# Kernel tuning notes

Hardware: AMD Instinct MI355X
Metric: run time of the kernel (lower is better)

The kernel has to match this reference:

```python
import jax, jax.numpy as jnp
import numpy as np

N, L, HID = 8192, 256, 128   # rows, input_len, hidden_size
H, NLIN = 2, 2               # n_heads, n_linear
EPS = 1e-5


def setup_inputs() -> dict:
    key = jax.random.key(0)
    ks = jax.random.split(key, 8)
    # attention params (torch.randn in source; scaled 0.02 for numerical sanity of softmax logits)
    Q = jax.random.normal(ks[0], (H, L, HID), jnp.float32) * 0.02
    K = jax.random.normal(ks[1], (H, L, HID), jnp.float32) * 0.02
    V_down = jax.random.normal(ks[2], (H, L, HID), jnp.float32) * 0.02
    V_up = jax.random.normal(ks[3], (H, HID, L), jnp.float32) * 0.02
    # nn.Linear(input_len, input_len): uniform(-1/sqrt(L), 1/sqrt(L))
    bnd = 1.0 / np.sqrt(L)
    W = jax.random.uniform(ks[4], (NLIN, L, L), jnp.float32, -bnd, bnd)
    b = jax.random.uniform(ks[5], (NLIN, L), jnp.float32, -bnd, bnd)
    x = jax.random.normal(ks[6], (N, L), jnp.float32)
    return {"x": x, "Q": Q, "K": K, "V_down": V_down, "V_up": V_up, "W": W, "b": b}


def _batch_norm(z):
    # custom BatchNorm1d: per-feature normalization over the batch (row) dim, no affine
    m = jnp.mean(z, axis=0, keepdims=True)
    v = jnp.var(z, axis=0, keepdims=True)
    return (z - m) * jax.lax.rsqrt(v + EPS)


def reference(x, Q, K, V_down, V_up, W, b):
    h = _batch_norm(x)                              # [N, L]
    dE = jnp.zeros_like(h)
    for i in range(Q.shape[0]):                     # small fixed head count
        q = h @ Q[i]                                # [N, HID]
        k = h @ K[i]                                # [N, HID]
        A = jax.nn.softmax(q @ k.T, axis=1)         # [N, N]
        dE = dE + A @ (h @ V_down[i]) @ V_up[i]     # low-rank value path
    h = _batch_norm(h + dE)
    for j in range(W.shape[0]):                     # per-row Linear+ReLU loop == batched matmul
        h = jax.nn.relu(h @ W[j].T + b[j])
    return h
```

## Files before the change

### kernel.cpp

```cpp
#include <hip/hip_runtime.h>
#include <hip/hip_bf16.h>

constexpr int Nrows = 8192;
constexpr int L     = 256;
constexpr int D     = 128;
constexpr float EPS = 1e-5f;

typedef __bf16 bf16x8 __attribute__((ext_vector_type(8)));
typedef __bf16 bf16x4 __attribute__((ext_vector_type(4)));
typedef float  f32x4  __attribute__((ext_vector_type(4)));

#define MFMA16(a, b, c) __builtin_amdgcn_mfma_f32_16x16x32_bf16((a), (b), (c), 0, 0, 0)

__global__ void k_cvt_params(const float* __restrict__ Q, const float* __restrict__ K,
                             const float* __restrict__ Vd, const float* __restrict__ Vup,
                             const float* __restrict__ W,
                             __bf16* __restrict__ Bt, __bf16* __restrict__ VupT,
                             __bf16* __restrict__ Wb) {
    int i = blockIdx.x * 256 + threadIdx.x;
    if (i < 6 * 128 * 256) {
        int g = i >> 15; int r = i & 32767; int d = r >> 8; int l = r & 255;
        const float* src = (g % 3 == 0 ? Q : (g % 3 == 1 ? K : Vd)) + (g / 3) * (L * D);
        Bt[i] = (__bf16)src[l * D + d];
    } else if (i < 8 * 128 * 256) {
        int j = i - 6 * 128 * 256;
        int h = j >> 15; int r = j & 32767; int l = r >> 7; int d = r & 127;
        VupT[j] = (__bf16)Vup[h * (D * L) + d * L + l];
    } else {
        int j = i - 8 * 128 * 256;
        Wb[j] = (__bf16)W[j];
    }
}

__global__ void k_bn_stats(const float* __restrict__ x, float* __restrict__ sum,
                           float* __restrict__ sq) {
    int col = threadIdx.x;
    int r0 = blockIdx.x * 64;
    float s = 0.f, s2 = 0.f;
    for (int i = 0; i < 64; i++) {
        float v = x[(r0 + i) * L + col];
        s += v; s2 += v * v;
    }
    atomicAdd(&sum[col], s);
    atomicAdd(&sq[col], s2);
}

__global__ void k_bn_norm1(const float* __restrict__ x, const float* __restrict__ sum,
                           const float* __restrict__ sq, __bf16* __restrict__ hb,
                           float* __restrict__ hf) {
    int i = (blockIdx.x * 256 + threadIdx.x) * 4;
    int col = i & (L - 1);
    f32x4 v = *(const f32x4*)(x + i);
    bf16x4 o; f32x4 of;
#pragma unroll
    for (int j = 0; j < 4; j++) {
        float m   = sum[col + j] * (1.0f / Nrows);
        float var = sq[col + j] * (1.0f / Nrows) - m * m;
        float rs  = rsqrtf(var + EPS);
        float t = (v[j] - m) * rs;
        of[j] = t; o[j] = (__bf16)t;
    }
    *(bf16x4*)(hb + i) = o;
    *(f32x4*)(hf + i) = of;
}

__global__ void k_bn_norm2(const float* __restrict__ z, const float* __restrict__ sum,
                           const float* __restrict__ sq, __bf16* __restrict__ h) {
    int i = (blockIdx.x * 256 + threadIdx.x) * 4;
    int col = i & (L - 1);
    f32x4 v = *(const f32x4*)(z + i);
    bf16x4 o;
#pragma unroll
    for (int j = 0; j < 4; j++) {
        float m   = sum[col + j] * (1.0f / Nrows);
        float var = sq[col + j] * (1.0f / Nrows) - m * m;
        float rs  = rsqrtf(var + EPS);
        o[j] = (__bf16)((v[j] - m) * rs);
    }
    *(bf16x4*)(h + i) = o;
}

__launch_bounds__(256)
__global__ void k_gemm_qkv(const __bf16* __restrict__ h, const __bf16* __restrict__ Bt,
                           __bf16* __restrict__ q0, __bf16* __restrict__ k0,
                           __bf16* __restrict__ q1, __bf16* __restrict__ k1,
                           __bf16* __restrict__ Vt) {
    int g = blockIdx.y;
    int m0 = blockIdx.x * 128;
    int w = threadIdx.x >> 6, lane = threadIdx.x & 63;
    int c = lane & 15, qd = lane >> 4;
    int mw = m0 + w * 32;
    const __bf16* B = Bt + g * (128 * 256);

    f32x4 acc[2][8] = {};
#pragma unroll
    for (int kc = 0; kc < 8; kc++) {
        bf16x8 a0 = *(const bf16x8*)(h + (mw + c) * L + kc * 32 + qd * 8);
        bf16x8 a1 = *(const bf16x8*)(h + (mw + 16 + c) * L + kc * 32 + qd * 8);
#pragma unroll
        for (int nt = 0; nt < 8; nt++) {
            bf16x8 b = *(const bf16x8*)(B + (nt * 16 + c) * L + kc * 32 + qd * 8);
            acc[0][nt] = MFMA16(a0, b, acc[0][nt]);
            acc[1][nt] = MFMA16(a1, b, acc[1][nt]);
        }
    }
    if (g == 2 || g == 5) {
        __bf16* vt = Vt + (g / 3) * (128 * Nrows);
#pragma unroll
        for (int mt = 0; mt < 2; mt++)
#pragma unroll
            for (int nt = 0; nt < 8; nt++)
#pragma unroll
                for (int r = 0; r < 4; r++) {
                    int row = mw + mt * 16 + 4 * qd + r;
                    int colv = nt * 16 + c;
                    vt[colv * Nrows + row] = (__bf16)acc[mt][nt][r];
                }
    } else {
        __bf16* dst = (g == 0) ? q0 : (g == 1) ? k0 : (g == 3) ? q1 : k1;
#pragma unroll
        for (int mt = 0; mt < 2; mt++)
#pragma unroll
            for (int nt = 0; nt < 8; nt++)
#pragma unroll
                for (int r = 0; r < 4; r++) {
                    int row = mw + mt * 16 + 4 * qd + r;
                    int colv = nt * 16 + c;
                    dst[row * D + colv] = (__bf16)acc[mt][nt][r];
                }
    }
}

__launch_bounds__(256, 1)
__global__ void k_flash(const __bf16* __restrict__ q0, const __bf16* __restrict__ k0,
                        const __bf16* __restrict__ q1, const __bf16* __restrict__ k1,
                        const __bf16* __restrict__ Vt, __bf16* __restrict__ O) {
    int head = blockIdx.x & 1;
    int qtile = blockIdx.x >> 1;
    int m0 = qtile * 64;
    const __bf16* qm = head ? q1 : q0;
    const __bf16* km = head ? k1 : k0;
    const __bf16* vt = Vt + head * (128 * Nrows);
    __bf16* Og = O + head * (Nrows * D);

    int w = threadIdx.x >> 6, lane = threadIdx.x & 63;
    int c = lane & 15, qd = lane >> 4;

    __shared__ __bf16 Pb[4][64 * 56];
    __shared__ float l_red[4][64];
    __shared__ float l_inv[64];
    __shared__ float obuf[4][64][16];

    bf16x8 aq[4][4];
#pragma unroll
    for (int mt = 0; mt < 4; mt++)
#pragma unroll
        for (int kc = 0; kc < 4; kc++)
            aq[mt][kc] = *(const bf16x8*)(qm + (m0 + mt * 16 + c) * D + kc * 32 + qd * 8);

    f32x4 oacc[4][8] = {};
    float lp[4][4] = {};
    __bf16* Pw = &Pb[w][0];

    auto loadkv = [&](bf16x8 (&kb)[2][4], bf16x8 (&vb)[8], int n0) {
        int nb = n0 + w * 32;
#pragma unroll
        for (int nt = 0; nt < 2; nt++)
#pragma unroll
            for (int kc = 0; kc < 4; kc++)
                kb[nt][kc] = *(const bf16x8*)(km + (nb + nt * 16 + c) * D + kc * 32 + qd * 8);
#pragma unroll
        for (int dvt = 0; dvt < 8; dvt++)
            vb[dvt] = *(const bf16x8*)(vt + (dvt * 16 + c) * Nrows + nb + qd * 8);
    };

    auto compute = [&](const bf16x8 (&kb)[2][4], const bf16x8 (&vb)[8]) {
#pragma unroll
        for (int nt = 0; nt < 2; nt++) {
            f32x4 s[4] = {};
            __builtin_amdgcn_s_setprio(1);
#pragma unroll
            for (int kc = 0; kc < 4; kc++) {
#pragma unroll
                for (int mt = 0; mt < 4; mt++) s[mt] = MFMA16(aq[mt][kc], kb[nt][kc], s[mt]);
            }
            __builtin_amdgcn_s_setprio(0);
#pragma unroll
            for (int mt = 0; mt < 4; mt++)
#pragma unroll
                for (int r = 0; r < 4; r++) {
                    float e = __expf(s[mt][r]);
                    lp[mt][r] += e;
                    Pw[(mt * 16 + 4 * qd + r) * 56 + nt * 16 + c] = (__bf16)e;
                }
        }
        bf16x8 ap[4];
#pragma unroll
        for (int mt = 0; mt < 4; mt++)
            ap[mt] = *(const bf16x8*)(Pw + (mt * 16 + c) * 56 + qd * 8);
        __builtin_amdgcn_s_setprio(1);
#pragma unroll
        for (int dvt = 0; dvt < 8; dvt++) {
#pragma unroll
            for (int mt = 0; mt < 4; mt++) oacc[mt][dvt] = MFMA16(ap[mt], vb[dvt], oacc[mt][dvt]);
        }
        __builtin_amdgcn_s_setprio(0);
    };

    bf16x8 kbA[2][4], vbA[8], kbB[2][4], vbB[8];
    loadkv(kbA, vbA, 0);
    for (int n0 = 0; n0 < Nrows; n0 += 256) {
        loadkv(kbB, vbB, n0 + 128);
        compute(kbA, vbA);
        if (n0 + 256 < Nrows)
            loadkv(kbA, vbA, n0 + 256);
        compute(kbB, vbB);
    }

#pragma unroll
    for (int mt = 0; mt < 4; mt++)
#pragma unroll
        for (int r = 0; r < 4; r++) {
            float v = lp[mt][r];
            v += __shfl_xor(v, 1, 16);
            v += __shfl_xor(v, 2, 16);
            v += __shfl_xor(v, 4, 16);
            v += __shfl_xor(v, 8, 16);
            lp[mt][r] = v;
        }
    if (c == 0) {
#pragma unroll
        for (int mt = 0; mt < 4; mt++)
#pragma unroll
            for (int r = 0; r < 4; r++)
                l_red[w][mt * 16 + 4 * qd + r] = lp[mt][r];
    }
    __syncthreads();
    if (threadIdx.x < 64)
        l_inv[threadIdx.x] = 1.0f / (l_red[0][threadIdx.x] + l_red[1][threadIdx.x] +
                                     l_red[2][threadIdx.x] + l_red[3][threadIdx.x]);

    for (int dvt = 0; dvt < 8; dvt++) {
        __syncthreads();
#pragma unroll
        for (int mt = 0; mt < 4; mt++)
#pragma unroll
            for (int r = 0; r < 4; r++)
                obuf[w][mt * 16 + 4 * qd + r][c] = oacc[mt][dvt][r];
        __syncthreads();
        int t = threadIdx.x;
        int row = (t * 4) >> 4, col = (t * 4) & 15;
        f32x4 v = *(const f32x4*)&obuf[0][row][col];
        f32x4 v1 = *(const f32x4*)&obuf[1][row][col];
        f32x4 v2 = *(const f32x4*)&obuf[2][row][col];
        f32x4 v3 = *(const f32x4*)&obuf[3][row][col];
        float il = l_inv[row];
        bf16x4 o;
#pragma unroll
        for (int e = 0; e < 4; e++) o[e] = (__bf16)((v[e] + v1[e] + v2[e] + v3[e]) * il);
        *(bf16x4*)(Og + (m0 + row) * D + dvt * 16 + col) = o;
    }
}

__launch_bounds__(256)
__global__ void k_gemm_vup(const __bf16* __restrict__ O, const __bf16* __restrict__ VupT,
                           const float* __restrict__ hf, float* __restrict__ z) {
    int n0 = blockIdx.y * 128;
    int m0 = blockIdx.x * 128;
    int w = threadIdx.x >> 6, lane = threadIdx.x & 63;
    int c = lane & 15, qd = lane >> 4;
    int mw = m0 + w * 32;

    f32x4 acc[2][8] = {};
#pragma unroll
    for (int kc = 0; kc < 8; kc++) {
        const __bf16* Oh = O + (kc >> 2) * (Nrows * D);
        const __bf16* Vh = VupT + (kc >> 2) * (L * D);
        int ko = (kc & 3) * 32 + qd * 8;
        bf16x8 a0 = *(const bf16x8*)(Oh + (mw + c) * D + ko);
        bf16x8 a1 = *(const bf16x8*)(Oh + (mw + 16 + c) * D + ko);
#pragma unroll
        for (int nt = 0; nt < 8; nt++) {
            bf16x8 b = *(const bf16x8*)(Vh + (n0 + nt * 16 + c) * D + ko);
            acc[0][nt] = MFMA16(a0, b, acc[0][nt]);
            acc[1][nt] = MFMA16(a1, b, acc[1][nt]);
        }
    }
#pragma unroll
    for (int mt = 0; mt < 2; mt++)
#pragma unroll
        for (int nt = 0; nt < 8; nt++)
#pragma unroll
            for (int r = 0; r < 4; r++) {
                int row = mw + mt * 16 + 4 * qd + r;
                int col = n0 + nt * 16 + c;
                z[row * L + col] = acc[mt][nt][r] + hf[row * L + col];
            }
}

template <typename OutT>
__launch_bounds__(256)
__global__ void k_gemm_w(const __bf16* __restrict__ hin, const __bf16* __restrict__ W,
                         const float* __restrict__ bias, OutT* __restrict__ out) {
    int n0 = blockIdx.y * 128;
    int m0 = blockIdx.x * 128;
    int w = threadIdx.x >> 6, lane = threadIdx.x & 63;
    int c = lane & 15, qd = lane >> 4;
    int mw = m0 + w * 32;

    f32x4 acc[2][8] = {};
#pragma unroll
    for (int kc = 0; kc < 8; kc++) {
        bf16x8 a0 = *(const bf16x8*)(hin + (mw + c) * L + kc * 32 + qd * 8);
        bf16x8 a1 = *(const bf16x8*)(hin + (mw + 16 + c) * L + kc * 32 + qd * 8);
#pragma unroll
        for (int nt = 0; nt < 8; nt++) {
            bf16x8 b = *(const bf16x8*)(W + (n0 + nt * 16 + c) * L + kc * 32 + qd * 8);
            acc[0][nt] = MFMA16(a0, b, acc[0][nt]);
            acc[1][nt] = MFMA16(a1, b, acc[1][nt]);
        }
    }
#pragma unroll
    for (int mt = 0; mt < 2; mt++)
#pragma unroll
        for (int nt = 0; nt < 8; nt++) {
            int col = n0 + nt * 16 + c;
            float bv = bias[col];
#pragma unroll
            for (int r = 0; r < 4; r++) {
                int row = mw + mt * 16 + 4 * qd + r;
                float v = fmaxf(acc[mt][nt][r] + bv, 0.0f);
                out[row * L + col] = (OutT)v;
            }
        }
}

extern "C" void kernel_launch(void* const* d_in, const int* in_sizes, int n_in,
                              void* d_out, int out_size, void* d_ws, size_t ws_size,
                              hipStream_t stream) {
    (void)in_sizes; (void)n_in; (void)out_size; (void)ws_size;
    const float* x   = (const float*)d_in[0];
    const float* Q   = (const float*)d_in[1];
    const float* K   = (const float*)d_in[2];
    const float* Vd  = (const float*)d_in[3];
    const float* Vup = (const float*)d_in[4];
    const float* W   = (const float*)d_in[5];
    const float* b   = (const float*)d_in[6];
    float* out = (float*)d_out;

    char* ws = (char*)d_ws;
    size_t off = 0;
    auto alloc = [&](size_t bytes) -> void* {
        void* p = ws + off;
        off += (bytes + 255) & ~(size_t)255;
        return p;
    };
    float*  stats = (float*)alloc(4 * 256 * sizeof(float));
    __bf16* Bt    = (__bf16*)alloc(6 * 128 * 256 * 2);
    __bf16* VupT  = (__bf16*)alloc(2 * 256 * 128 * 2);
    __bf16* Wb    = (__bf16*)alloc(2 * 256 * 256 * 2);
    __bf16* hb    = (__bf16*)alloc((size_t)Nrows * L * 2);
    float*  hf    = (float*)alloc((size_t)Nrows * L * 4);
    __bf16* q0    = (__bf16*)alloc((size_t)Nrows * D * 2);
    __bf16* k0    = (__bf16*)alloc((size_t)Nrows * D * 2);
    __bf16* q1    = (__bf16*)alloc((size_t)Nrows * D * 2);
    __bf16* k1    = (__bf16*)alloc((size_t)Nrows * D * 2);
    __bf16* Vt    = (__bf16*)alloc((size_t)2 * 128 * Nrows * 2);
    __bf16* O     = (__bf16*)alloc((size_t)2 * Nrows * D * 2);
    float*  z     = (float*)alloc((size_t)Nrows * L * 4);
    __bf16* h2    = (__bf16*)alloc((size_t)Nrows * L * 2);
    __bf16* h3    = (__bf16*)alloc((size_t)Nrows * L * 2);

    float* sum1 = stats, *sq1 = stats + 256, *sum2 = stats + 512, *sq2 = stats + 768;

    hipMemsetAsync(stats, 0, 4 * 256 * sizeof(float), stream);
    k_cvt_params<<<1536, 256, 0, stream>>>(Q, K, Vd, Vup, W, Bt, VupT, Wb);
    k_bn_stats<<<128, 256, 0, stream>>>(x, sum1, sq1);
    k_bn_norm1<<<2048, 256, 0, stream>>>(x, sum1, sq1, hb, hf);
    k_gemm_qkv<<<dim3(64, 6), 256, 0, stream>>>(hb, Bt, q0, k0, q1, k1, Vt);
    k_flash<<<256, 256, 0, stream>>>(q0, k0, q1, k1, Vt, O);
    k_gemm_vup<<<dim3(64, 2), 256, 0, stream>>>(O, VupT, hf, z);
    k_bn_stats<<<128, 256, 0, stream>>>(z, sum2, sq2);
    k_bn_norm2<<<2048, 256, 0, stream>>>(z, sum2, sq2, h2);
    k_gemm_w<__bf16><<<dim3(64, 2), 256, 0, stream>>>(h2, Wb, b, h3);
    k_gemm_w<float><<<dim3(64, 2), 256, 0, stream>>>(h3, Wb + 256 * 256, b + 256, out);
}
```

Baseline: 306.0 us.

## Keep softmax probabilities in registers via transposed QK^T and K16 MFMA for PV

Restructures the attention kernel so S^T is computed as K·Q^T, whose accumulator layout matches the B operand of a 16x16x16 bf16 MFMA. The exponentiated probabilities then feed the PV product straight from registers instead of making a round trip through shared memory. Work is split across 8 waves, each owning 16 query rows and half of every 64-key chunk, and the two halves are reduced in shared memory at the end. This removes the LDS write/read of P, but each wave reloads K/V for fewer query rows (less reuse per load) and uses a smaller-K MFMA.

```diff
diff --git a/kernel.cpp b/kernel.cpp
--- a/kernel.cpp
+++ b/kernel.cpp
@@ -9,8 +9,15 @@
 typedef __bf16 bf16x8 __attribute__((ext_vector_type(8)));
 typedef __bf16 bf16x4 __attribute__((ext_vector_type(4)));
 typedef float  f32x4  __attribute__((ext_vector_type(4)));
+typedef short  s16x4  __attribute__((ext_vector_type(4)));
 
 #define MFMA16(a, b, c) __builtin_amdgcn_mfma_f32_16x16x32_bf16((a), (b), (c), 0, 0, 0)
+
+#if __has_builtin(__builtin_amdgcn_mfma_f32_16x16x16bf16_1k)
+#define MFMA_K16(A_, B_, C_) (C_) = __builtin_amdgcn_mfma_f32_16x16x16bf16_1k((A_), (B_), (C_), 0, 0, 0)
+#else
+#define MFMA_K16(A_, B_, C_) asm volatile("s_nop 1\n\tv_mfma_f32_16x16x16_bf16 %0, %1, %2, %0" : "+v"(C_) : "v"(A_), "v"(B_))
+#endif
 
 __global__ void k_cvt_params(const float* __restrict__ Q, const float* __restrict__ K,
                              const float* __restrict__ Vd, const float* __restrict__ Vup,
@@ -131,7 +138,7 @@
     }
 }
 
-__launch_bounds__(256, 1)
+__launch_bounds__(512, 1)
 __global__ void k_flash(const __bf16* __restrict__ q0, const __bf16* __restrict__ k0,
                         const __bf16* __restrict__ q1, const __bf16* __restrict__ k1,
                         const __bf16* __restrict__ Vt, __bf16* __restrict__ O) {
@@ -143,122 +150,92 @@
     const __bf16* vt = Vt + head * (128 * Nrows);
     __bf16* Og = O + head * (Nrows * D);
 
-    int w = threadIdx.x >> 6, lane = threadIdx.x & 63;
+    int w = threadIdx.x >> 6;
+    int qh = w >> 1;
+    int ks = w & 1;
+    int lane = threadIdx.x & 63;
     int c = lane & 15, qd = lane >> 4;
-
-    __shared__ __bf16 Pb[4][64 * 56];
-    __shared__ float l_red[4][64];
-    __shared__ float l_inv[64];
-    __shared__ float obuf[4][64][16];
-
-    bf16x8 aq[4][4];
-#pragma unroll
-    for (int mt = 0; mt < 4; mt++)
-#pragma unroll
-        for (int kc = 0; kc < 4; kc++)
-            aq[mt][kc] = *(const bf16x8*)(qm + (m0 + mt * 16 + c) * D + kc * 32 + qd * 8);
-
-    f32x4 oacc[4][8] = {};
-    float lp[4][4] = {};
-    __bf16* Pw = &Pb[w][0];
-
-    auto loadkv = [&](bf16x8 (&kb)[2][4], bf16x8 (&vb)[8], int n0) {
-        int nb = n0 + w * 32;
+    int mq = m0 + qh * 16;
+
+    __shared__ float obuf[4][16][136];
+    __shared__ float lred[8][16];
+
+    bf16x8 aq[4];
+#pragma unroll
+    for (int kc = 0; kc < 4; kc++)
+        aq[kc] = *(const bf16x8*)(qm + (mq + c) * D + kc * 32 + qd * 8);
+
+    f32x4 oacc[8] = {};
+    float lp = 0.f;
+
+    auto loadk = [&](bf16x8 (&kb)[2][4], int n0) {
+        int nb = n0 + ks * 32;
 #pragma unroll
         for (int nt = 0; nt < 2; nt++)
 #pragma unroll
             for (int kc = 0; kc < 4; kc++)
                 kb[nt][kc] = *(const bf16x8*)(km + (nb + nt * 16 + c) * D + kc * 32 + qd * 8);
+    };
+    auto loadv = [&](s16x4 (&vb)[8][2], int n0) {
+        int nb = n0 + ks * 32;
 #pragma unroll
         for (int dvt = 0; dvt < 8; dvt++)
-            vb[dvt] = *(const bf16x8*)(vt + (dvt * 16 + c) * Nrows + nb + qd * 8);
+#pragma unroll
+            for (int nt = 0; nt < 2; nt++)
+                vb[dvt][nt] = *(const s16x4*)(vt + (dvt * 16 + c) * Nrows + nb + nt * 16 + qd * 4);
     };
-
-    auto compute = [&](const bf16x8 (&kb)[2][4], const bf16x8 (&vb)[8]) {
+    auto compute = [&](const bf16x8 (&kb)[2][4], const s16x4 (&vb)[8][2]) {
 #pragma unroll
         for (int nt = 0; nt < 2; nt++) {
-            f32x4 s[4] = {};
+            f32x4 s = {};
             __builtin_amdgcn_s_setprio(1);
 #pragma unroll
-            for (int kc = 0; kc < 4; kc++) {
-#pragma unroll
-                for (int mt = 0; mt < 4; mt++) s[mt] = MFMA16(aq[mt][kc], kb[nt][kc], s[mt]);
-            }
+            for (int kc = 0; kc < 4; kc++) s = MFMA16(kb[nt][kc], aq[kc], s);
             __builtin_amdgcn_s_setprio(0);
-#pragma unroll
-            for (int mt = 0; mt < 4; mt++)
-#pragma unroll
-                for (int r = 0; r < 4; r++) {
-                    float e = __expf(s[mt][r]);
-                    lp[mt][r] += e;
-                    Pw[(mt * 16 + 4 * qd + r) * 56 + nt * 16 + c] = (__bf16)e;
-                }
-        }
-        bf16x8 ap[4];
-#pragma unroll
-        for (int mt = 0; mt < 4; mt++)
-            ap[mt] = *(const bf16x8*)(Pw + (mt * 16 + c) * 56 + qd * 8);
-        __builtin_amdgcn_s_setprio(1);
+            float e0 = __expf(s[0]), e1 = __expf(s[1]);
+            float e2 = __expf(s[2]), e3 = __expf(s[3]);
+            lp += (e0 + e1) + (e2 + e3);
+            bf16x4 pbv; pbv[0] = (__bf16)e0; pbv[1] = (__bf16)e1;
+            pbv[2] = (__bf16)e2; pbv[3] = (__bf16)e3;
+            s16x4 pb = __builtin_bit_cast(s16x4, pbv);
+            __builtin_amdgcn_s_setprio(1);
+#pragma unroll
+            for (int dvt = 0; dvt < 8; dvt++) MFMA_K16(vb[dvt][nt], pb, oacc[dvt]);
+            __builtin_amdgcn_s_setprio(0);
+        }
+    };
+
+    bf16x8 kbA[2][4], kbB[2][4];
+    s16x4  vbA[8][2], vbB[8][2];
+    loadk(kbA, 0); loadv(vbA, 0);
+    for (int n0 = 0; n0 < Nrows; n0 += 128) {
+        loadk(kbB, n0 + 64); loadv(vbB, n0 + 64);
+        compute(kbA, vbA);
+        if (n0 + 128 < Nrows) { loadk(kbA, n0 + 128); loadv(vbA, n0 + 128); }
+        compute(kbB, vbB);
+    }
+    asm volatile("s_nop 7\n\ts_nop 7" ::: "memory");
+
+    float lv = lp;
+    lv += __shfl_xor(lv, 16);
+    lv += __shfl_xor(lv, 32);
+    if (lane < 16) lred[w][lane] = lv;
+    if (ks == 1) {
+#pragma unroll
+        for (int dvt = 0; dvt < 8; dvt++)
+            *(f32x4*)&obuf[qh][c][dvt * 16 + qd * 4] = oacc[dvt];
+    }
+    __syncthreads();
+    if (ks == 0) {
+        float il = 1.0f / (lred[w][c] + lred[w + 1][c]);
 #pragma unroll
         for (int dvt = 0; dvt < 8; dvt++) {
-#pragma unroll
-            for (int mt = 0; mt < 4; mt++) oacc[mt][dvt] = MFMA16(ap[mt], vb[dvt], oacc[mt][dvt]);
-        }
-        __builtin_amdgcn_s_setprio(0);
-    };
-
-    bf16x8 kbA[2][4], vbA[8], kbB[2][4], vbB[8];
-    loadkv(kbA, vbA, 0);
-    for (int n0 = 0; n0 < Nrows; n0 += 256) {
-        loadkv(kbB, vbB, n0 + 128);
-        compute(kbA, vbA);
-        if (n0 + 256 < Nrows)
-            loadkv(kbA, vbA, n0 + 256);
-        compute(kbB, vbB);
-    }
-
-#pragma unroll
-    for (int mt = 0; mt < 4; mt++)
-#pragma unroll
-        for (int r = 0; r < 4; r++) {
-            float v = lp[mt][r];
-            v += __shfl_xor(v, 1, 16);
-            v += __shfl_xor(v, 2, 16);
-            v += __shfl_xor(v, 4, 16);
-            v += __shfl_xor(v, 8, 16);
-            lp[mt][r] = v;
-        }
-    if (c == 0) {
-#pragma unroll
-        for (int mt = 0; mt < 4; mt++)
-#pragma unroll
-            for (int r = 0; r < 4; r++)
-                l_red[w][mt * 16 + 4 * qd + r] = lp[mt][r];
-    }
-    __syncthreads();
-    if (threadIdx.x < 64)
-        l_inv[threadIdx.x] = 1.0f / (l_red[0][threadIdx.x] + l_red[1][threadIdx.x] +
-                                     l_red[2][threadIdx.x] + l_red[3][threadIdx.x]);
-
-    for (int dvt = 0; dvt < 8; dvt++) {
-        __syncthreads();
-#pragma unroll
-        for (int mt = 0; mt < 4; mt++)
-#pragma unroll
-            for (int r = 0; r < 4; r++)
-                obuf[w][mt * 16 + 4 * qd + r][c] = oacc[mt][dvt][r];
-        __syncthreads();
-        int t = threadIdx.x;
-        int row = (t * 4) >> 4, col = (t * 4) & 15;
-        f32x4 v = *(const f32x4*)&obuf[0][row][col];
-        f32x4 v1 = *(const f32x4*)&obuf[1][row][col];
-        f32x4 v2 = *(const f32x4*)&obuf[2][row][col];
-        f32x4 v3 = *(const f32x4*)&obuf[3][row][col];
-        float il = l_inv[row];
-        bf16x4 o;
-#pragma unroll
-        for (int e = 0; e < 4; e++) o[e] = (__bf16)((v[e] + v1[e] + v2[e] + v3[e]) * il);
-        *(bf16x4*)(Og + (m0 + row) * D + dvt * 16 + col) = o;
+            f32x4 v = oacc[dvt] + *(const f32x4*)&obuf[qh][c][dvt * 16 + qd * 4];
+            bf16x4 o;
+#pragma unroll
+            for (int e = 0; e < 4; e++) o[e] = (__bf16)(v[e] * il);
+            *(bf16x4*)(Og + (mq + c) * D + dvt * 16 + qd * 4) = o;
+        }
     }
 }
 
@@ -378,7 +355,7 @@
     k_bn_stats<<<128, 256, 0, stream>>>(x, sum1, sq1);
     k_bn_norm1<<<2048, 256, 0, stream>>>(x, sum1, sq1, hb, hf);
     k_gemm_qkv<<<dim3(64, 6), 256, 0, stream>>>(hb, Bt, q0, k0, q1, k1, Vt);
-    k_flash<<<256, 256, 0, stream>>>(q0, k0, q1, k1, Vt, O);
+    k_flash<<<256, 512, 0, stream>>>(q0, k0, q1, k1, Vt, O);
     k_gemm_vup<<<dim3(64, 2), 256, 0, stream>>>(O, VupT, hf, z);
     k_bn_stats<<<128, 256, 0, stream>>>(z, sum2, sq2);
     k_bn_norm2<<<2048, 256, 0, stream>>>(z, sum2, sq2, h2);
```

Result: slower. 855.8 us (+179.7%).

## Software-pipeline flash attention: overlap QK/exp of next tile with PV MFMA

Applied to the files above, without the earlier changes.

Splits the per-tile compute into QK+exp, P readback, and PV matmul stages. It double-buffers the P tile in shared memory so the QK/exp of the next key tile is issued before the PV MFMAs of the previous one. The goal is to hide exp/LDS latency behind matrix work and keep the MFMA units busy. This doubles the P shared-memory footprint and extends register live ranges, which could hurt occupancy or scheduling.

```diff
diff --git a/kernel.cpp b/kernel.cpp
--- a/kernel.cpp
+++ b/kernel.cpp
@@ -146,7 +146,7 @@
     int w = threadIdx.x >> 6, lane = threadIdx.x & 63;
     int c = lane & 15, qd = lane >> 4;
 
-    __shared__ __bf16 Pb[4][64 * 56];
+    __shared__ __bf16 Pb[2][4][64 * 56];
     __shared__ float l_red[4][64];
     __shared__ float l_inv[64];
     __shared__ float obuf[4][64][16];
@@ -160,7 +160,8 @@
 
     f32x4 oacc[4][8] = {};
     float lp[4][4] = {};
-    __bf16* Pw = &Pb[w][0];
+    __bf16* Pw0 = &Pb[0][w][0];
+    __bf16* Pw1 = &Pb[1][w][0];
 
     auto loadkv = [&](bf16x8 (&kb)[2][4], bf16x8 (&vb)[8], int n0) {
         int nb = n0 + w * 32;
@@ -174,7 +175,7 @@
             vb[dvt] = *(const bf16x8*)(vt + (dvt * 16 + c) * Nrows + nb + qd * 8);
     };
 
-    auto compute = [&](const bf16x8 (&kb)[2][4], const bf16x8 (&vb)[8]) {
+    auto qkexp = [&](const bf16x8 (&kb)[2][4], __bf16* Pw) {
 #pragma unroll
         for (int nt = 0; nt < 2; nt++) {
             f32x4 s[4] = {};
@@ -194,10 +195,13 @@
                     Pw[(mt * 16 + 4 * qd + r) * 56 + nt * 16 + c] = (__bf16)e;
                 }
         }
-        bf16x8 ap[4];
+    };
+    auto readp = [&](bf16x8 (&ap)[4], const __bf16* Pw) {
 #pragma unroll
         for (int mt = 0; mt < 4; mt++)
             ap[mt] = *(const bf16x8*)(Pw + (mt * 16 + c) * 56 + qd * 8);
+    };
+    auto pvm = [&](const bf16x8 (&ap)[4], const bf16x8 (&vb)[8]) {
         __builtin_amdgcn_s_setprio(1);
 #pragma unroll
         for (int dvt = 0; dvt < 8; dvt++) {
@@ -207,15 +211,25 @@
         __builtin_amdgcn_s_setprio(0);
     };
 
-    bf16x8 kbA[2][4], vbA[8], kbB[2][4], vbB[8];
+    bf16x8 kbA[2][4], vbA[8], kbB[2][4], vbB[8], ap[4];
     loadkv(kbA, vbA, 0);
-    for (int n0 = 0; n0 < Nrows; n0 += 256) {
+    qkexp(kbA, Pw0);
+    loadkv(kbB, vbB, 128);
+    for (int n0 = 256; n0 < Nrows; n0 += 256) {
+        readp(ap, Pw0);
+        qkexp(kbB, Pw1);
+        pvm(ap, vbA);
+        loadkv(kbA, vbA, n0);
+        readp(ap, Pw1);
+        qkexp(kbA, Pw0);
+        pvm(ap, vbB);
         loadkv(kbB, vbB, n0 + 128);
-        compute(kbA, vbA);
-        if (n0 + 256 < Nrows)
-            loadkv(kbA, vbA, n0 + 256);
-        compute(kbB, vbB);
-    }
+    }
+    readp(ap, Pw0);
+    qkexp(kbB, Pw1);
+    pvm(ap, vbA);
+    readp(ap, Pw1);
+    pvm(ap, vbB);
 
 #pragma unroll
     for (int mt = 0; mt < 4; mt++)
```

New measurement: 588.6 us. 92.3% more time.
